# Optimization experiments

Measured on AMD Instinct MI355X. Metric: run time of the kernel, lower is better.

Reference implementation:

```python
import jax, jax.numpy as jnp
import numpy as np

EPS = 1e-5

def _bn(x, g, b, m, v):
    # inference-mode batchnorm with moving statistics
    return (x - m) * jax.lax.rsqrt(v + EPS) * g + b

def setup_inputs() -> dict:
    key = jax.random.key(0)
    ks = jax.random.split(key, 12)
    t, b, s, hu = 512, 64, 1024, 1024
    d_in = s + hu
    si = jax.random.normal(ks[0], (b, s), dtype=jnp.float32)
    h = jax.random.normal(ks[1], (t, b, hu), dtype=jnp.float32)
    W0 = jax.random.normal(ks[2], (d_in, 10), dtype=jnp.float32) * 0.02
    b0 = jnp.zeros((10,), jnp.float32)
    g0 = jnp.ones((10,), jnp.float32)
    be0 = jnp.zeros((10,), jnp.float32)
    m0 = jax.random.normal(ks[3], (10,), dtype=jnp.float32) * 0.1
    v0 = jax.random.uniform(ks[4], (10,), dtype=jnp.float32) + 0.5
    W1 = jax.random.normal(ks[5], (10, 5), dtype=jnp.float32) * 0.3
    b1 = jnp.zeros((5,), jnp.float32)
    g1 = jnp.ones((5,), jnp.float32)
    be1 = jnp.zeros((5,), jnp.float32)
    m1 = jax.random.normal(ks[6], (5,), dtype=jnp.float32) * 0.1
    v1 = jax.random.uniform(ks[7], (5,), dtype=jnp.float32) + 0.5
    W2 = jax.random.normal(ks[8], (5, 1), dtype=jnp.float32) * 0.4
    b2 = jnp.zeros((1,), jnp.float32)
    return {"si": si, "h": h, "W0": W0, "b0": b0, "g0": g0, "be0": be0,
            "m0": m0, "v0": v0, "W1": W1, "b1": b1, "g1": g1, "be1": be1,
            "m1": m1, "v1": v1, "W2": W2, "b2": b2}

def reference(si, h, W0, b0, g0, be0, m0, v0, W1, b1, g1, be1, m1, v1, W2, b2):
    t, b, hu = h.shape
    # concat decoder state with every encoder hidden state: [t, b, s+hu]
    x = jnp.concatenate([jnp.broadcast_to(si[None], (t,) + si.shape), h], axis=-1)
    x = jax.nn.relu(_bn(x @ W0 + b0, g0, be0, m0, v0))
    x = jax.nn.relu(_bn(x @ W1 + b1, g1, be1, m1, v1))
    scores = x @ W2 + b2                       # [t, b, 1]
    # original: tf.concat over axis 0 -> [t*b, 1], softmax over axis 0 (ALL t*b entries)
    a = jax.nn.softmax(scores.reshape(t * b))  # [t*b]
    # original uses only the first t rows of the flattened softmax as scalar weights
    ci = jnp.einsum('t,tbh->bh', a[:t], h)     # [b, hu]
    return ci
```

## Files before the change

### kernel.cpp

```cpp
#include <hip/hip_runtime.h>

#define EPS 1e-5f

constexpr int T  = 512;
constexpr int B  = 64;
constexpr int HU = 1024;
constexpr int S  = 1024;
constexpr int C  = B * HU;
constexpr int NSLAB = 64;

constexpr size_t OFF_SIW0 = 0;
constexpr size_t OFF_W    = 1024;
constexpr size_t OFF_ESC  = 2048;
constexpr size_t OFF_W0T  = 34816;
constexpr size_t OFF_PART = 45056;

__device__ __forceinline__ float mlp_head(
    const float* __restrict__ u10,
    const float* __restrict__ b0, const float* __restrict__ g0,
    const float* __restrict__ be0,const float* __restrict__ m0,
    const float* __restrict__ v0,
    const float* __restrict__ W1, const float* __restrict__ b1,
    const float* __restrict__ g1, const float* __restrict__ be1,
    const float* __restrict__ m1, const float* __restrict__ v1,
    const float* __restrict__ W2, const float* __restrict__ b2) {
    float y[10];
#pragma unroll
    for (int j = 0; j < 10; ++j) {
        float u = (u10[j] + b0[j] - m0[j]) * (1.0f / sqrtf(v0[j] + EPS)) * g0[j]
                  + be0[j];
        y[j] = fmaxf(u, 0.f);
    }
    float z[5];
#pragma unroll
    for (int i = 0; i < 5; ++i) {
        float u = b1[i];
#pragma unroll
        for (int j = 0; j < 10; ++j) u = fmaf(y[j], W1[j * 5 + i], u);
        u = (u - m1[i]) * (1.0f / sqrtf(v1[i] + EPS)) * g1[i] + be1[i];
        z[i] = fmaxf(u, 0.f);
    }
    float sc = b2[0];
#pragma unroll
    for (int i = 0; i < 5; ++i) sc = fmaf(z[i], W2[i], sc);
    return sc;
}

__global__ __launch_bounds__(1024) void k_tr(const float* __restrict__ W0,
                                             float* __restrict__ W0T) {
    const int k = threadIdx.x;
    const float* src = W0 + (size_t)(1024 + k) * 10;
    float v[10];
#pragma unroll
    for (int q = 0; q < 5; ++q) {
        const float2 p = ((const float2*)src)[q];
        v[2 * q] = p.x; v[2 * q + 1] = p.y;
    }
#pragma unroll
    for (int j = 0; j < 10; ++j) W0T[j * 1024 + k] = v[j];
}

__global__ __launch_bounds__(256) void k_weights(
    const float* __restrict__ h,  const float* __restrict__ si,
    const float* __restrict__ W0,
    const float* __restrict__ b0, const float* __restrict__ g0,
    const float* __restrict__ be0,const float* __restrict__ m0,
    const float* __restrict__ v0,
    const float* __restrict__ W1, const float* __restrict__ b1,
    const float* __restrict__ g1, const float* __restrict__ be1,
    const float* __restrict__ m1, const float* __restrict__ v1,
    const float* __restrict__ W2, const float* __restrict__ b2,
    float* __restrict__ w, float* __restrict__ siW0out) {
    const int e   = blockIdx.x;
    const int t   = e >> 6;
    const int cb  = e & 63;
    const int tid = threadIdx.x;
    const int wv  = tid >> 6, ln = tid & 63;

    const float4 hv = *(const float4*)(h  + (size_t)t  * C + (size_t)cb * HU + tid * 4);
    const float4 sv = *(const float4*)(si + (size_t)cb * S + tid * 4);
    const float* wsb = W0 + (size_t)(4 * tid) * 10;
    const float* whb = W0 + (size_t)(1024 + 4 * tid) * 10;

    float ssi[10], shh[10];
#pragma unroll
    for (int j = 0; j < 10; ++j) { ssi[j] = 0.f; shh[j] = 0.f; }
#pragma unroll
    for (int d = 0; d < 4; ++d) {
        const float sx = (&sv.x)[d], hx = (&hv.x)[d];
#pragma unroll
        for (int j = 0; j < 10; ++j) {
            ssi[j] = fmaf(sx, wsb[d * 10 + j], ssi[j]);
            shh[j] = fmaf(hx, whb[d * 10 + j], shh[j]);
        }
    }
#pragma unroll
    for (int j = 0; j < 10; ++j) {
#pragma unroll
        for (int off = 32; off > 0; off >>= 1) {
            ssi[j] += __shfl_down(ssi[j], off, 64);
            shh[j] += __shfl_down(shh[j], off, 64);
        }
    }
    __shared__ float rs[4][10], rh[4][10];
    if (ln == 0) {
#pragma unroll
        for (int j = 0; j < 10; ++j) { rs[wv][j] = ssi[j]; rh[wv][j] = shh[j]; }
    }
    __syncthreads();

    if (t == 0 && tid < 10)
        siW0out[cb * 10 + tid] = rs[0][tid] + rs[1][tid] + rs[2][tid] + rs[3][tid];

    if (tid == 0) {
        float u10[10];
#pragma unroll
        for (int j = 0; j < 10; ++j)
            u10[j] = rs[0][j] + rs[1][j] + rs[2][j] + rs[3][j] +
                     rh[0][j] + rh[1][j] + rh[2][j] + rh[3][j];
        const float sc = mlp_head(u10, b0, g0, be0, m0, v0,
                                  W1, b1, g1, be1, m1, v1, W2, b2);
        w[t * 64 + cb] = expf(sc);
    }
}

__global__ __launch_bounds__(256, 4) void k_stream(
    const float* __restrict__ h,  const float* __restrict__ W0T,
    const float* __restrict__ w,  const float* __restrict__ siW0,
    const float* __restrict__ b0, const float* __restrict__ g0,
    const float* __restrict__ be0,const float* __restrict__ m0,
    const float* __restrict__ v0,
    const float* __restrict__ W1, const float* __restrict__ b1,
    const float* __restrict__ g1, const float* __restrict__ be1,
    const float* __restrict__ m1, const float* __restrict__ v1,
    const float* __restrict__ W2, const float* __restrict__ b2,
    float* __restrict__ escore, float* __restrict__ part) {
    const int b    = blockIdx.x & 63;
    const int tg   = blockIdx.x >> 6;
    const int wv   = threadIdx.x >> 6;
    const int ln   = threadIdx.x & 63;
    const int t0   = tg * 32 + wv * 8;
    const int slab = tg * 4 + wv;

    float acc[16];
#pragma unroll
    for (int s = 0; s < 16; ++s) acc[s] = 0.f;

#pragma unroll
    for (int pass = 0; pass < 2; ++pass) {
        const int tA = t0 + pass * 4;
        const float* hp = h + ((size_t)tA * 64 + b) * HU;
        const float wt0 = w[tA + 0], wt1 = w[tA + 1];
        const float wt2 = w[tA + 2], wt3 = w[tA + 3];

        float sacc[4][10];
#pragma unroll
        for (int r = 0; r < 4; ++r)
#pragma unroll
            for (int j = 0; j < 10; ++j) sacc[r][j] = 0.f;

#pragma unroll 4
        for (int s = 0; s < 16; ++s) {
            const int k = 64 * s + ln;
            float w0t[10];
#pragma unroll
            for (int j = 0; j < 10; ++j) w0t[j] = W0T[j * 1024 + k];

            const float hx0 = hp[k];
            const float hx1 = hp[(size_t)1 * 64 * HU + k];
            const float hx2 = hp[(size_t)2 * 64 * HU + k];
            const float hx3 = hp[(size_t)3 * 64 * HU + k];
#pragma unroll
            for (int j = 0; j < 10; ++j) {
                sacc[0][j] = fmaf(hx0, w0t[j], sacc[0][j]);
                sacc[1][j] = fmaf(hx1, w0t[j], sacc[1][j]);
                sacc[2][j] = fmaf(hx2, w0t[j], sacc[2][j]);
                sacc[3][j] = fmaf(hx3, w0t[j], sacc[3][j]);
            }
            acc[s] = fmaf(wt0, hx0, acc[s]);
            acc[s] = fmaf(wt1, hx1, acc[s]);
            acc[s] = fmaf(wt2, hx2, acc[s]);
            acc[s] = fmaf(wt3, hx3, acc[s]);
        }

#pragma unroll
        for (int r = 0; r < 4; ++r) {
            float u10[10];
#pragma unroll
            for (int j = 0; j < 10; ++j) {
                float v = sacc[r][j];
#pragma unroll
                for (int off = 32; off > 0; off >>= 1)
                    v += __shfl_xor(v, off, 64);
                u10[j] = v + siW0[b * 10 + j];
            }
            const float sc = mlp_head(u10, b0, g0, be0, m0, v0,
                                      W1, b1, g1, be1, m1, v1, W2, b2);
            if (ln == 0)
                escore[(size_t)(tA + r) * 64 + b] = expf(sc);
        }
    }

    float* pp = part + (size_t)slab * C + (size_t)b * HU;
#pragma unroll
    for (int s = 0; s < 16; ++s) pp[64 * s + ln] = acc[s];
}

__global__ __launch_bounds__(256) void k_out(const float* __restrict__ part,
                                             const float* __restrict__ escore,
                                             float* __restrict__ out) {
    const int tid = threadIdx.x;
    const int wv  = tid >> 6, ln = tid & 63;

    float zs = 0.f;
#pragma unroll
    for (int q = 0; q < 32; ++q) {
        const float4 v = ((const float4*)escore)[tid + 256 * q];
        zs += v.x + v.y + v.z + v.w;
    }
#pragma unroll
    for (int off = 32; off > 0; off >>= 1)
        zs += __shfl_down(zs, off, 64);
    __shared__ float zr[4];
    __shared__ float sinv;
    if (ln == 0) zr[wv] = zs;
    __syncthreads();
    if (tid == 0) sinv = 1.0f / (zr[0] + zr[1] + zr[2] + zr[3]);
    __syncthreads();
    const float invZ = sinv;

    const int c = blockIdx.x * 1024 + tid * 4;
    float4 s = {0.f, 0.f, 0.f, 0.f};
#pragma unroll 8
    for (int sl = 0; sl < NSLAB; ++sl) {
        const float4 v = *(const float4*)(part + (size_t)sl * C + c);
        s.x += v.x; s.y += v.y; s.z += v.z; s.w += v.w;
    }
    s.x *= invZ; s.y *= invZ; s.z *= invZ; s.w *= invZ;
    *(float4*)(out + c) = s;
}

extern "C" void kernel_launch(void* const* d_in, const int* in_sizes, int n_in,
                              void* d_out, int out_size, void* d_ws, size_t ws_size,
                              hipStream_t stream) {
    const float* si  = (const float*)d_in[0];
    const float* h   = (const float*)d_in[1];
    const float* W0  = (const float*)d_in[2];
    const float* b0  = (const float*)d_in[3];
    const float* g0  = (const float*)d_in[4];
    const float* be0 = (const float*)d_in[5];
    const float* m0  = (const float*)d_in[6];
    const float* v0  = (const float*)d_in[7];
    const float* W1  = (const float*)d_in[8];
    const float* b1  = (const float*)d_in[9];
    const float* g1  = (const float*)d_in[10];
    const float* be1 = (const float*)d_in[11];
    const float* m1  = (const float*)d_in[12];
    const float* v1  = (const float*)d_in[13];
    const float* W2  = (const float*)d_in[14];
    const float* b2  = (const float*)d_in[15];

    float* ws     = (float*)d_ws;
    float* siW0   = ws + OFF_SIW0;
    float* w      = ws + OFF_W;
    float* escore = ws + OFF_ESC;
    float* W0T    = ws + OFF_W0T;
    float* part   = ws + OFF_PART;
    float* out    = (float*)d_out;

    hipLaunchKernelGGL(k_tr,      dim3(1),    dim3(1024), 0, stream, W0, W0T);
    hipLaunchKernelGGL(k_weights, dim3(512),  dim3(256),  0, stream, h, si, W0,
                       b0, g0, be0, m0, v0, W1, b1, g1, be1, m1, v1, W2, b2,
                       w, siW0);
    hipLaunchKernelGGL(k_stream,  dim3(1024), dim3(256),  0, stream, h, W0T, w,
                       siW0, b0, g0, be0, m0, v0, W1, b1, g1, be1, m1, v1,
                       W2, b2, escore, part);
    hipLaunchKernelGGL(k_out,     dim3(64),   dim3(256),  0, stream, part,
                       escore, out);
}
```

Baseline: 288.4 us.

## Halve per-wave timestep work, double stream grid and partial slabs, use float2 loads

The streaming kernel now gives each wave 4 timesteps instead of 8, launching 2048 blocks and writing 128 partial slabs instead of 64. Loads of h and the transposed W0 switch to float2, and the occupancy hint is removed from launch_bounds. The aim is more parallelism and wider memory transactions over the large h read. In exchange the partial-sum buffer doubles, which adds write traffic in the stream kernel and read traffic in the final reduction kernel.

```diff
diff --git a/kernel.cpp b/kernel.cpp
--- a/kernel.cpp
+++ b/kernel.cpp
@@ -7,7 +7,7 @@
 constexpr int HU = 1024;
 constexpr int S  = 1024;
 constexpr int C  = B * HU;
-constexpr int NSLAB = 64;
+constexpr int NSLAB = 128;
 
 constexpr size_t OFF_SIW0 = 0;
 constexpr size_t OFF_W    = 1024;
@@ -124,7 +124,7 @@
     }
 }
 
-__global__ __launch_bounds__(256, 4) void k_stream(
+__global__ __launch_bounds__(256) void k_stream(
     const float* __restrict__ h,  const float* __restrict__ W0T,
     const float* __restrict__ w,  const float* __restrict__ siW0,
     const float* __restrict__ b0, const float* __restrict__ g0,
@@ -139,71 +139,72 @@
     const int tg   = blockIdx.x >> 6;
     const int wv   = threadIdx.x >> 6;
     const int ln   = threadIdx.x & 63;
-    const int t0   = tg * 32 + wv * 8;
+    const int t0   = tg * 16 + wv * 4;
     const int slab = tg * 4 + wv;
 
-    float acc[16];
-#pragma unroll
-    for (int s = 0; s < 16; ++s) acc[s] = 0.f;
-
-#pragma unroll
-    for (int pass = 0; pass < 2; ++pass) {
-        const int tA = t0 + pass * 4;
-        const float* hp = h + ((size_t)tA * 64 + b) * HU;
-        const float wt0 = w[tA + 0], wt1 = w[tA + 1];
-        const float wt2 = w[tA + 2], wt3 = w[tA + 3];
-
-        float sacc[4][10];
-#pragma unroll
-        for (int r = 0; r < 4; ++r)
-#pragma unroll
-            for (int j = 0; j < 10; ++j) sacc[r][j] = 0.f;
+    const float* hp = h + ((size_t)t0 * 64 + b) * HU;
+    const float wt0 = w[t0 + 0], wt1 = w[t0 + 1];
+    const float wt2 = w[t0 + 2], wt3 = w[t0 + 3];
+
+    float2 acc[8];
+#pragma unroll
+    for (int s = 0; s < 8; ++s) { acc[s].x = 0.f; acc[s].y = 0.f; }
+    float sacc[4][10];
+#pragma unroll
+    for (int r = 0; r < 4; ++r)
+#pragma unroll
+        for (int j = 0; j < 10; ++j) sacc[r][j] = 0.f;
 
 #pragma unroll 4
-        for (int s = 0; s < 16; ++s) {
-            const int k = 64 * s + ln;
-            float w0t[10];
-#pragma unroll
-            for (int j = 0; j < 10; ++j) w0t[j] = W0T[j * 1024 + k];
-
-            const float hx0 = hp[k];
-            const float hx1 = hp[(size_t)1 * 64 * HU + k];
-            const float hx2 = hp[(size_t)2 * 64 * HU + k];
-            const float hx3 = hp[(size_t)3 * 64 * HU + k];
-#pragma unroll
-            for (int j = 0; j < 10; ++j) {
-                sacc[0][j] = fmaf(hx0, w0t[j], sacc[0][j]);
-                sacc[1][j] = fmaf(hx1, w0t[j], sacc[1][j]);
-                sacc[2][j] = fmaf(hx2, w0t[j], sacc[2][j]);
-                sacc[3][j] = fmaf(hx3, w0t[j], sacc[3][j]);
-            }
-            acc[s] = fmaf(wt0, hx0, acc[s]);
-            acc[s] = fmaf(wt1, hx1, acc[s]);
-            acc[s] = fmaf(wt2, hx2, acc[s]);
-            acc[s] = fmaf(wt3, hx3, acc[s]);
-        }
-
-#pragma unroll
-        for (int r = 0; r < 4; ++r) {
-            float u10[10];
-#pragma unroll
-            for (int j = 0; j < 10; ++j) {
-                float v = sacc[r][j];
-#pragma unroll
-                for (int off = 32; off > 0; off >>= 1)
-                    v += __shfl_xor(v, off, 64);
-                u10[j] = v + siW0[b * 10 + j];
-            }
-            const float sc = mlp_head(u10, b0, g0, be0, m0, v0,
-                                      W1, b1, g1, be1, m1, v1, W2, b2);
-            if (ln == 0)
-                escore[(size_t)(tA + r) * 64 + b] = expf(sc);
-        }
+    for (int s = 0; s < 8; ++s) {
+        const int k2 = 64 * s + ln;
+        float2 w0t[10];
+#pragma unroll
+        for (int j = 0; j < 10; ++j)
+            w0t[j] = ((const float2*)(W0T + (size_t)j * 1024))[k2];
+
+        const float2 h0 = ((const float2*)hp)[k2];
+        const float2 h1 = ((const float2*)(hp + (size_t)1 * 64 * HU))[k2];
+        const float2 h2 = ((const float2*)(hp + (size_t)2 * 64 * HU))[k2];
+        const float2 h3 = ((const float2*)(hp + (size_t)3 * 64 * HU))[k2];
+
+#pragma unroll
+        for (int j = 0; j < 10; ++j) {
+            sacc[0][j] = fmaf(h0.x, w0t[j].x, sacc[0][j]);
+            sacc[0][j] = fmaf(h0.y, w0t[j].y, sacc[0][j]);
+            sacc[1][j] = fmaf(h1.x, w0t[j].x, sacc[1][j]);
+            sacc[1][j] = fmaf(h1.y, w0t[j].y, sacc[1][j]);
+            sacc[2][j] = fmaf(h2.x, w0t[j].x, sacc[2][j]);
+            sacc[2][j] = fmaf(h2.y, w0t[j].y, sacc[2][j]);
+            sacc[3][j] = fmaf(h3.x, w0t[j].x, sacc[3][j]);
+            sacc[3][j] = fmaf(h3.y, w0t[j].y, sacc[3][j]);
+        }
+        acc[s].x = fmaf(wt0, h0.x, acc[s].x); acc[s].y = fmaf(wt0, h0.y, acc[s].y);
+        acc[s].x = fmaf(wt1, h1.x, acc[s].x); acc[s].y = fmaf(wt1, h1.y, acc[s].y);
+        acc[s].x = fmaf(wt2, h2.x, acc[s].x); acc[s].y = fmaf(wt2, h2.y, acc[s].y);
+        acc[s].x = fmaf(wt3, h3.x, acc[s].x); acc[s].y = fmaf(wt3, h3.y, acc[s].y);
     }
 
     float* pp = part + (size_t)slab * C + (size_t)b * HU;
 #pragma unroll
-    for (int s = 0; s < 16; ++s) pp[64 * s + ln] = acc[s];
+    for (int s = 0; s < 8; ++s) ((float2*)pp)[64 * s + ln] = acc[s];
+
+#pragma unroll
+    for (int r = 0; r < 4; ++r) {
+        float u10[10];
+#pragma unroll
+        for (int j = 0; j < 10; ++j) {
+            float v = sacc[r][j];
+#pragma unroll
+            for (int off = 32; off > 0; off >>= 1)
+                v += __shfl_xor(v, off, 64);
+            u10[j] = v + siW0[b * 10 + j];
+        }
+        const float sc = mlp_head(u10, b0, g0, be0, m0, v0,
+                                  W1, b1, g1, be1, m1, v1, W2, b2);
+        if (ln == 0)
+            escore[(size_t)(t0 + r) * 64 + b] = expf(sc);
+    }
 }
 
 __global__ __launch_bounds__(256) void k_out(const float* __restrict__ part,
@@ -272,7 +273,7 @@
     hipLaunchKernelGGL(k_weights, dim3(512),  dim3(256),  0, stream, h, si, W0,
                        b0, g0, be0, m0, v0, W1, b1, g1, be1, m1, v1, W2, b2,
                        w, siW0);
-    hipLaunchKernelGGL(k_stream,  dim3(1024), dim3(256),  0, stream, h, W0T, w,
+    hipLaunchKernelGGL(k_stream,  dim3(2048), dim3(256),  0, stream, h, W0T, w,
                        siW0, b0, g0, be0, m0, v0, W1, b1, g1, be1, m1, v1,
                        W2, b2, escore, part);
     hipLaunchKernelGGL(k_out,     dim3(64),   dim3(256),  0, stream, part,
```

Result: slower. 326.2 us (+13.1%).
